# Optimization experiments

Measured on AMD Instinct MI355X. Metric: run time of the kernel, lower is better.

Reference implementation:

```python
import jax, jax.numpy as jnp
import numpy as np
import math

B, H, S, DK = 4, 16, 2048, 64

def setup_inputs() -> dict:
    key = jax.random.key(0)
    kq, kk, kv, km = jax.random.split(key, 4)
    q = jax.random.normal(kq, (B, H, S, DK), dtype=jnp.float32)
    k = jax.random.normal(kk, (B, H, S, DK), dtype=jnp.float32)
    v = jax.random.normal(kv, (B, H, S, DK), dtype=jnp.float32)
    mask = jax.random.randint(km, (B, 1, 1, S), 0, 2, dtype=jnp.int32)
    return {"q": q, "k": k, "v": v, "mask": mask}

def reference(q, k, v, mask):
    scale = 1.0 / math.sqrt(DK)
    # scores: [B, H, S, S]
    scores = jnp.einsum('bhqd,bhkd->bhqk', q, k) * scale
    scores = jnp.where(mask == 0, jnp.float32(-1e9), scores)
    attn = jax.nn.softmax(scores, axis=-1)
    out = jnp.einsum('bhqk,bhkd->bhqd', attn, v)
    return out
```

## Files before the change

### kernel.cpp

```cpp
#include <hip/hip_runtime.h>
#include <hip/hip_bf16.h>

#define S_LEN 2048
#define D_K   64
#define N_H   16
#define N_B   4
#define KVB   64
#define QPB   256
#define NQB   (S_LEN / QPB)
#define NBH   (N_B * N_H)
#define WS_NEED (2L * NBH * S_LEN * D_K * 2 + 4L * S_LEN * 4 + 16)

typedef __attribute__((ext_vector_type(8)))  short bf16x8;
typedef __attribute__((ext_vector_type(16))) float f32x16;
typedef unsigned int u32;
typedef __attribute__((ext_vector_type(4))) u32 u32x4;

__device__ inline short f2bfs(float x) {
    __hip_bfloat16 h = __float2bfloat16(x);
    return __builtin_bit_cast(short, h);
}

__device__ inline bf16x8 cvt8(const float* __restrict__ p) {
    float4 a = *(const float4*)p;
    float4 b = *(const float4*)(p + 4);
    bf16x8 f;
    f[0] = f2bfs(a.x); f[1] = f2bfs(a.y);
    f[2] = f2bfs(a.z); f[3] = f2bfs(a.w);
    f[4] = f2bfs(b.x); f[5] = f2bfs(b.y);
    f[6] = f2bfs(b.z); f[7] = f2bfs(b.w);
    return f;
}

__device__ inline bf16x8 cvt8s(const float* __restrict__ p, float s) {
    float4 a = *(const float4*)p;
    float4 b = *(const float4*)(p + 4);
    bf16x8 f;
    f[0] = f2bfs(a.x * s); f[1] = f2bfs(a.y * s);
    f[2] = f2bfs(a.z * s); f[3] = f2bfs(a.w * s);
    f[4] = f2bfs(b.x * s); f[5] = f2bfs(b.y * s);
    f[6] = f2bfs(b.z * s); f[7] = f2bfs(b.w * s);
    return f;
}

__device__ inline int vswz(int d) { return ((d & 7) ^ ((d >> 3) & 7)) << 4; }

__device__ inline void gld16(const void* g, void* l) {
    __builtin_amdgcn_global_load_lds(
        (const __attribute__((address_space(1))) void*)g,
        (__attribute__((address_space(3))) void*)l, 16, 0, 0);
}

__global__ __launch_bounds__(64)
void mask_scan(const int* __restrict__ mask, int* __restrict__ idx,
               int* __restrict__ cnt) {
    const int b = blockIdx.x, lane = threadIdx.x;
    const int* mb = mask + b * S_LEN;
    int base = 0;
    for (int j0 = 0; j0 < S_LEN; j0 += 64) {
        int mv = mb[j0 + lane];
        unsigned long long ball = __ballot(mv != 0);
        int pos = base + __popcll(ball & ((1ull << lane) - 1ull));
        if (mv) idx[b * S_LEN + pos] = j0 + lane;
        base += __popcll(ball);
    }
    if (lane == 0) cnt[b] = base;
}

__global__ __launch_bounds__(256)
void gather_cvt(const float* __restrict__ k, const float* __restrict__ v,
                const int* __restrict__ idx, const int* __restrict__ cnt,
                short* __restrict__ kc, short* __restrict__ vt) {
    const int bid = blockIdx.x, bh = bid >> 5, i0 = (bid & 31) * 64;
    const int b = bh >> 4;
    const int m = cnt[b];
    if (i0 >= ((m + 63) & ~63)) return;
    const int t = threadIdx.x;
    const int r = t >> 2, c0 = (t & 3) * 16;
    const int i = i0 + r;

    __shared__ __align__(16) short tile_[64][72];
    bf16x8 fv0, fv1, fk0, fk1;
    if (i < m) {
        const int src = idx[b * S_LEN + i];
        const float* kp = k + ((long)bh * S_LEN + src) * D_K + c0;
        const float* vp = v + ((long)bh * S_LEN + src) * D_K + c0;
        fk0 = cvt8(kp); fk1 = cvt8(kp + 8);
        fv0 = cvt8(vp); fv1 = cvt8(vp + 8);
    } else {
#pragma unroll
        for (int j = 0; j < 8; ++j) { fk0[j] = 0; fk1[j] = 0; fv0[j] = 0; fv1[j] = 0; }
    }
    short* kdst = kc + ((long)bh * S_LEN + i) * D_K + c0;
    *(bf16x8*)kdst       = fk0;
    *(bf16x8*)(kdst + 8) = fk1;
    *(bf16x8*)&tile_[r][c0]     = fv0;
    *(bf16x8*)&tile_[r][c0 + 8] = fv1;
    __syncthreads();
    const int dd = t >> 2, k0 = (t & 3) * 16;
    bf16x8 h0, h1;
#pragma unroll
    for (int j = 0; j < 8; ++j) {
        h0[j] = tile_[k0 + j][dd];
        h1[j] = tile_[k0 + 8 + j][dd];
    }
    short* dst = vt + ((long)bh * D_K + dd) * S_LEN + i0 + k0;
    *(bf16x8*)dst       = h0;
    *(bf16x8*)(dst + 8) = h1;
}

__global__ __launch_bounds__(512)
void attn_fwd(const float* __restrict__ q, const short* __restrict__ kbf,
              const short* __restrict__ vtb, const int* __restrict__ cnt,
              float* __restrict__ out) {
    const int id      = blockIdx.x;
    const int logical = (id & 7) * 64 + (id >> 3);
    const int bh      = logical >> 3;
    const int qblk    = logical & 7;
    const int b       = bh >> 4;
    const int t       = threadIdx.x;
    const int lane    = t & 63;
    const int wq      = t >> 6;
    const int hb      = lane >> 5;
    const int ql      = lane & 31;

    const int m   = cnt[b];
    const int NTr = (m + 63) >> 6;

    __shared__ __align__(16) short kbuf[5][KVB * D_K];
    __shared__ __align__(16) short vbuf[4][D_K * KVB];

    const float scale2 = 0.125f * 1.44269504f;
    const long  baseq  = (long)bh * S_LEN * D_K;
    const int   qrow0  = qblk * QPB + wq * 32;

    bf16x8 qf[4];
    {
        const float* qp = q + baseq + (long)(qrow0 + ql) * D_K + hb * 8;
#pragma unroll
        for (int kd = 0; kd < 4; ++kd) qf[kd] = cvt8s(qp + kd * 16, scale2);
    }

    const int lrow = lane >> 3, lchk = lane & 7;
    const int rA = wq * 8 + lrow;
    const short* ksA = kbf + baseq + (long)rA * D_K + ((lchk ^ (rA & 7)) * 8);
    const short* vsA = vtb + ((long)bh * D_K + rA) * S_LEN
                       + ((lchk ^ ((rA & 7) ^ ((rA >> 3) & 7))) * 8);

    auto STAGE_K = [&](int i) {
        gld16(ksA + (long)i * (KVB * D_K),
              (char*)kbuf + (i % 5) * (KVB * D_K * 2) + (wq * 8) * 128);
    };
    auto STAGE_V = [&](int i) {
        gld16(vsA + (long)i * KVB,
              (char*)vbuf + (i % 4) * (D_K * KVB * 2) + (wq * 8) * 128);
    };

    f32x16 o0, o1;
#pragma unroll
    for (int r = 0; r < 16; ++r) { o0[r] = 0.f; o1[r] = 0.f; }
    float lrun = 0.f;

    f32x16 ZEROV;
#pragma unroll
    for (int r = 0; r < 16; ++r) ZEROV[r] = 0.f;

    f32x16 st0, st1;

    auto QK = [&](int kv0, int sel, bool lastt) {
        const char* kbp = (const char*)kbuf + sel * (KVB * D_K * 2);
        int rb0 = (ql) * 128,      sz0 = (ql & 7) << 4;
        int rb1 = (32 + ql) * 128;
        f32x16 a0, a1;
        __builtin_amdgcn_s_setprio(1);
        {
            int co = (hb * 8) * 2;
            bf16x8 kf0 = *(const bf16x8*)(kbp + ((rb0 + co) ^ sz0));
            bf16x8 kf1 = *(const bf16x8*)(kbp + ((rb1 + co) ^ sz0));
            if (!lastt) {
                a0 = __builtin_amdgcn_mfma_f32_32x32x16_bf16(kf0, qf[0], ZEROV, 0, 0, 0);
                a1 = __builtin_amdgcn_mfma_f32_32x32x16_bf16(kf1, qf[0], ZEROV, 0, 0, 0);
            } else {
                f32x16 c0, c1;
                int keyb = kv0 + 4 * hb;
#pragma unroll
                for (int r = 0; r < 16; ++r) {
                    int key = keyb + (r & 3) + 8 * (r >> 2);
                    c0[r] = (key < m)      ? 0.f : -1e9f;
                    c1[r] = (key + 32 < m) ? 0.f : -1e9f;
                }
                a0 = __builtin_amdgcn_mfma_f32_32x32x16_bf16(kf0, qf[0], c0, 0, 0, 0);
                a1 = __builtin_amdgcn_mfma_f32_32x32x16_bf16(kf1, qf[0], c1, 0, 0, 0);
            }
        }
#pragma unroll
        for (int kd = 1; kd < 4; ++kd) {
            int co = (kd * 16 + hb * 8) * 2;
            bf16x8 kf0 = *(const bf16x8*)(kbp + ((rb0 + co) ^ sz0));
            bf16x8 kf1 = *(const bf16x8*)(kbp + ((rb1 + co) ^ sz0));
            a0 = __builtin_amdgcn_mfma_f32_32x32x16_bf16(kf0, qf[kd], a0, 0, 0, 0);
            a1 = __builtin_amdgcn_mfma_f32_32x32x16_bf16(kf1, qf[kd], a1, 0, 0, 0);
        }
        __builtin_amdgcn_s_setprio(0);
        st0 = a0; st1 = a1;
    };

    u32 w[2][8];

    auto SM = [&]() {
        float rs0 = 0.f, rs1 = 0.f;
#pragma unroll
        for (int mm = 0; mm < 8; ++mm) {
            float p0 = __builtin_amdgcn_exp2f(st0[2 * mm]);
            float p1 = __builtin_amdgcn_exp2f(st0[2 * mm + 1]);
            rs0 += p0; rs1 += p1;
            u32 r;
            asm("v_cvt_pk_bf16_f32 %0, %1, %2" : "=v"(r) : "v"(p0), "v"(p1));
            w[0][mm] = r;
        }
#pragma unroll
        for (int mm = 0; mm < 8; ++mm) {
            float p0 = __builtin_amdgcn_exp2f(st1[2 * mm]);
            float p1 = __builtin_amdgcn_exp2f(st1[2 * mm + 1]);
            rs0 += p0; rs1 += p1;
            u32 r;
            asm("v_cvt_pk_bf16_f32 %0, %1, %2" : "=v"(r) : "v"(p0), "v"(p1));
            w[1][mm] = r;
        }
        float rs = rs0 + rs1;
        rs += __shfl_xor(rs, 32, 64);
        lrun += rs;
    };

    auto PV = [&](int sel) {
        const char* vbp = (const char*)vbuf + sel * (D_K * KVB * 2);
#pragma unroll
        for (int kbi = 0; kbi < 4; ++kbi) {
            int c = kbi >> 1, a2 = (kbi & 1) * 4;
            u32 x0 = w[c][a2 + 0], y0 = w[c][a2 + 2];
            u32 x1 = w[c][a2 + 1], y1 = w[c][a2 + 3];
            asm("v_permlane32_swap_b32 %0, %1" : "+v"(x0), "+v"(y0));
            asm("v_permlane32_swap_b32 %0, %1" : "+v"(x1), "+v"(y1));
            u32x4 av = {x0, x1, y0, y1};
            bf16x8 pa = __builtin_bit_cast(bf16x8, av);
            __builtin_amdgcn_s_setprio(1);
#pragma unroll
            for (int dn = 0; dn < 2; ++dn) {
                int d = dn * 32 + ql;
                bf16x8 vf = *(const bf16x8*)(vbp +
                              ((d * 128 + (kbi * 16 + hb * 8) * 2) ^ vswz(d)));
                if (dn == 0)
                    o0 = __builtin_amdgcn_mfma_f32_32x32x16_bf16(pa, vf, o0, 0, 0, 0);
                else
                    o1 = __builtin_amdgcn_mfma_f32_32x32x16_bf16(pa, vf, o1, 0, 0, 0);
            }
            __builtin_amdgcn_s_setprio(0);
        }
    };

    STAGE_K(0);
    STAGE_V(0);
    if (NTr > 1) { STAGE_K(1); STAGE_V(1); }
    if (NTr > 2) STAGE_K(2);
    if (NTr > 3) STAGE_K(3);
    __syncthreads();
    QK(0, 0, NTr == 1);
    __syncthreads();

    for (int u = 0; 2 * u < NTr; ++u) {
        const int t0 = 2 * u, t1 = 2 * u + 1;
        if (t0 + 4 < NTr) STAGE_K(t0 + 4);
        if (t0 + 5 < NTr) STAGE_K(t0 + 5);
        if (t0 + 2 < NTr) STAGE_V(t0 + 2);
        if (t0 + 3 < NTr) STAGE_V(t0 + 3);

        SM();
        if (t0 + 1 < NTr) QK((t0 + 1) * KVB, (t0 + 1) % 5, t0 + 2 == NTr);
        PV(t0 & 3);

        if (t1 < NTr) {
            SM();
            if (t1 + 1 < NTr) QK((t1 + 1) * KVB, (t1 + 1) % 5, t1 + 2 == NTr);
            PV(t1 & 3);
        }

        __syncthreads();
    }

    float rl = 1.0f / lrun;
#pragma unroll
    for (int r = 0; r < 16; ++r) {
        int   cr  = (r & 3) + 8 * (r >> 2) + 4 * hb;
        float rlr = __shfl(rl, cr, 64);
        long  rowb = baseq + (long)(qrow0 + cr) * D_K;
        out[rowb + ql]      = o0[r] * rlr;
        out[rowb + 32 + ql] = o1[r] * rlr;
    }
}

__global__ __launch_bounds__(256)
void attn_fwd_legacy(const float* __restrict__ q, const float* __restrict__ k,
                     const float* __restrict__ v, const int* __restrict__ mask,
                     float* __restrict__ out) {
    const int id      = blockIdx.x;
    const int logical = (id & 7) * 128 + (id >> 3);
    const int bh      = logical >> 4;
    const int qblk    = logical & 15;
    const int b       = bh >> 4;
    const int t       = threadIdx.x;
    const int lane    = t & 63;
    const int wq      = t >> 6;
    const int hb      = lane >> 5;
    const int ql      = lane & 31;

    __shared__ __align__(16) short kbuf[KVB * D_K];
    __shared__ __align__(16) short vtbuf[D_K * KVB];
    __shared__ float mbias[S_LEN];

    const float scale2 = 0.125f * 1.44269504f;
    const long  base   = (long)bh * S_LEN * D_K;
    const int   qrow0  = qblk * 128 + wq * 32;

    {
        const int* mb = mask + b * S_LEN;
        for (int i = t; i < S_LEN; i += 256)
            mbias[i] = mb[i] ? 0.f : -1.442695e9f;
    }

    bf16x8 qf[4];
    {
        const float* qp = q + base + (long)(qrow0 + ql) * D_K + hb * 8;
#pragma unroll
        for (int kd = 0; kd < 4; ++kd) qf[kd] = cvt8s(qp + kd * 16, 1.0f);
    }

    f32x16 o0, o1;
#pragma unroll
    for (int r = 0; r < 16; ++r) { o0[r] = 0.f; o1[r] = 0.f; }
    float mrun = -1e30f, lrun = 0.f;

    const int srow = t >> 3;
    const int scol = t & 7;
    float4 kr[2][2], vr[2][2];

    auto LOADT = [&](int kv0) {
#pragma unroll
        for (int u2 = 0; u2 < 2; ++u2) {
            int row = srow + u2 * 32;
            const float* kp = k + base + (long)(kv0 + row) * D_K + scol * 8;
            const float* vp = v + base + (long)(kv0 + row) * D_K + scol * 8;
            kr[u2][0] = *(const float4*)kp; kr[u2][1] = *(const float4*)(kp + 4);
            vr[u2][0] = *(const float4*)vp; vr[u2][1] = *(const float4*)(vp + 4);
        }
    };

    LOADT(0);

    for (int tt = 0; tt < S_LEN / KVB; ++tt) {
        const int kv0 = tt * KVB;
        __syncthreads();
#pragma unroll
        for (int u2 = 0; u2 < 2; ++u2) {
            int row = srow + u2 * 32;
            bf16x8 fk, fv;
#pragma unroll
            for (int j = 0; j < 4; ++j) {
                fk[j]     = f2bfs(((const float*)&kr[u2][0])[j]);
                fk[j + 4] = f2bfs(((const float*)&kr[u2][1])[j]);
                fv[j]     = f2bfs(((const float*)&vr[u2][0])[j]);
                fv[j + 4] = f2bfs(((const float*)&vr[u2][1])[j]);
            }
            int kbyte = (row * 128 + scol * 16) ^ ((row & 7) << 4);
            *(bf16x8*)((char*)kbuf + kbyte) = fk;
#pragma unroll
            for (int j = 0; j < 8; ++j) {
                int d = scol * 8 + j;
                *(short*)((char*)vtbuf + ((d * 128 + row * 2) ^ vswz(d))) = fv[j];
            }
        }
        if (tt + 1 < S_LEN / KVB) LOADT(kv0 + KVB);
        __syncthreads();

        f32x16 stl[2];
#pragma unroll
        for (int kb32 = 0; kb32 < 2; ++kb32) {
            f32x16 acc;
#pragma unroll
            for (int r = 0; r < 16; ++r) acc[r] = 0.f;
            int krow = kb32 * 32 + ql;
            int rb = krow * 128, sz = (krow & 7) << 4;
#pragma unroll
            for (int kd = 0; kd < 4; ++kd) {
                bf16x8 kf = *(const bf16x8*)((const char*)kbuf + ((rb + (kd * 16 + hb * 8) * 2) ^ sz));
                acc = __builtin_amdgcn_mfma_f32_32x32x16_bf16(kf, qf[kd], acc, 0, 0, 0);
            }
            stl[kb32] = acc;
        }
#pragma unroll
        for (int kb32 = 0; kb32 < 2; ++kb32)
#pragma unroll
            for (int r = 0; r < 16; ++r) {
                int key = kv0 + kb32 * 32 + (r & 3) + 8 * (r >> 2) + 4 * hb;
                stl[kb32][r] = fmaf(stl[kb32][r], scale2, mbias[key]);
            }

        float m8[8];
#pragma unroll
        for (int i = 0; i < 8; ++i)
            m8[i] = fmaxf(fmaxf(stl[0][i], stl[0][i + 8]),
                          fmaxf(stl[1][i], stl[1][i + 8]));
        float tmax = fmaxf(fmaxf(fmaxf(m8[0], m8[1]), fmaxf(m8[2], m8[3])),
                           fmaxf(fmaxf(m8[4], m8[5]), fmaxf(m8[6], m8[7])));
        tmax = fmaxf(tmax, __shfl_xor(tmax, 32, 64));

        if (__any(tmax > mrun + 10.0f)) {
            float mnew = fmaxf(mrun, tmax);
            float al   = __builtin_amdgcn_exp2f(mrun - mnew);
            mrun = mnew;
            lrun *= al;
#pragma unroll
            for (int r = 0; r < 16; ++r) {
                float ar = __shfl(al, (r & 3) + 8 * (r >> 2) + 4 * hb, 64);
                o0[r] *= ar; o1[r] *= ar;
            }
        }

        u32 w[2][8];
        float rs = 0.f;
#pragma unroll
        for (int kb32 = 0; kb32 < 2; ++kb32)
#pragma unroll
            for (int mm = 0; mm < 8; ++mm) {
                float p0 = __builtin_amdgcn_exp2f(stl[kb32][2 * mm]     - mrun);
                float p1 = __builtin_amdgcn_exp2f(stl[kb32][2 * mm + 1] - mrun);
                rs += p0 + p1;
                w[kb32][mm] = (u32)(unsigned short)f2bfs(p0) |
                              ((u32)(unsigned short)f2bfs(p1) << 16);
            }
        rs += __shfl_xor(rs, 32, 64);
        lrun += rs;

#pragma unroll
        for (int kbi = 0; kbi < 4; ++kbi) {
            int c = kbi >> 1, a2 = (kbi & 1) * 4;
            u32 x0 = w[c][a2 + 0], y0 = w[c][a2 + 2];
            u32 x1 = w[c][a2 + 1], y1 = w[c][a2 + 3];
            asm("v_permlane32_swap_b32 %0, %1" : "+v"(x0), "+v"(y0));
            asm("v_permlane32_swap_b32 %0, %1" : "+v"(x1), "+v"(y1));
            u32x4 av = {x0, x1, y0, y1};
            bf16x8 pa = __builtin_bit_cast(bf16x8, av);
#pragma unroll
            for (int dn = 0; dn < 2; ++dn) {
                int d = dn * 32 + ql;
                bf16x8 vf = *(const bf16x8*)((const char*)vtbuf +
                              ((d * 128 + (kbi * 16 + hb * 8) * 2) ^ vswz(d)));
                if (dn == 0)
                    o0 = __builtin_amdgcn_mfma_f32_32x32x16_bf16(pa, vf, o0, 0, 0, 0);
                else
                    o1 = __builtin_amdgcn_mfma_f32_32x32x16_bf16(pa, vf, o1, 0, 0, 0);
            }
        }
    }

    float rl = 1.0f / lrun;
#pragma unroll
    for (int r = 0; r < 16; ++r) {
        int   cr  = (r & 3) + 8 * (r >> 2) + 4 * hb;
        float rlr = __shfl(rl, cr, 64);
        long  rowb = base + (long)(qrow0 + cr) * D_K;
        out[rowb + ql]      = o0[r] * rlr;
        out[rowb + 32 + ql] = o1[r] * rlr;
    }
}

extern "C" void kernel_launch(void* const* d_in, const int* in_sizes, int n_in,
                              void* d_out, int out_size, void* d_ws, size_t ws_size,
                              hipStream_t stream) {
    const float* q    = (const float*)d_in[0];
    const float* k    = (const float*)d_in[1];
    const float* v    = (const float*)d_in[2];
    const int*   mask = (const int*)d_in[3];
    float*       out  = (float*)d_out;

    if (ws_size >= (size_t)WS_NEED) {
        short* kc  = (short*)d_ws;
        short* vt  = kc + (long)NBH * S_LEN * D_K;
        int*   idx = (int*)(vt + (long)NBH * S_LEN * D_K);
        int*   cnt = idx + 4 * S_LEN;
        mask_scan<<<dim3(N_B), 64, 0, stream>>>(mask, idx, cnt);
        gather_cvt<<<dim3(NBH * (S_LEN / 64)), 256, 0, stream>>>(k, v, idx, cnt, kc, vt);
        attn_fwd<<<dim3(NQB * NBH), 512, 0, stream>>>(q, kc, vt, cnt, out);
    } else {
        attn_fwd_legacy<<<dim3((S_LEN / 128) * NBH), 256, 0, stream>>>(q, k, v, mask, out);
    }
}
```

Measured before the change: 80.80 us.

## Fuse mask compaction scan into gather kernel and defer row-sum shuffle

Removes the separate single-wave-per-batch mask_scan launch. Each gather_cvt block now rescans the mask itself and keeps only the 64 compacted indices it needs in shared memory. This saves a kernel launch and a serial dependency, at the cost of every block redundantly reading 2048 mask ints. Separately, the softmax row-sum cross-half shuffle is moved out of the per-tile loop and done once at the end.

```diff
diff --git a/kernel.cpp b/kernel.cpp
--- a/kernel.cpp
+++ b/kernel.cpp
@@ -51,38 +51,44 @@
         (__attribute__((address_space(3))) void*)l, 16, 0, 0);
 }
 
-__global__ __launch_bounds__(64)
-void mask_scan(const int* __restrict__ mask, int* __restrict__ idx,
-               int* __restrict__ cnt) {
-    const int b = blockIdx.x, lane = threadIdx.x;
-    const int* mb = mask + b * S_LEN;
-    int base = 0;
-    for (int j0 = 0; j0 < S_LEN; j0 += 64) {
-        int mv = mb[j0 + lane];
-        unsigned long long ball = __ballot(mv != 0);
-        int pos = base + __popcll(ball & ((1ull << lane) - 1ull));
-        if (mv) idx[b * S_LEN + pos] = j0 + lane;
-        base += __popcll(ball);
-    }
-    if (lane == 0) cnt[b] = base;
-}
-
 __global__ __launch_bounds__(256)
 void gather_cvt(const float* __restrict__ k, const float* __restrict__ v,
-                const int* __restrict__ idx, const int* __restrict__ cnt,
-                short* __restrict__ kc, short* __restrict__ vt) {
+                const int* __restrict__ mask, const int dummy,
+                short* __restrict__ kc, short* __restrict__ vt,
+                int* __restrict__ cnt) {
     const int bid = blockIdx.x, bh = bid >> 5, i0 = (bid & 31) * 64;
     const int b = bh >> 4;
-    const int m = cnt[b];
+    const int t = threadIdx.x;
+
+    __shared__ __align__(16) short tile_[64][72];
+    __shared__ int idx_s[64];
+    __shared__ int m_s;
+
+    if (t < 64) {
+        const int lane = t;
+        const int* mb = mask + b * S_LEN;
+        int base = 0;
+#pragma unroll 4
+        for (int j0 = 0; j0 < S_LEN; j0 += 64) {
+            int mv = mb[j0 + lane];
+            unsigned long long ball = __ballot(mv != 0);
+            int pos = base + __popcll(ball & ((1ull << lane) - 1ull));
+            if (mv && pos >= i0 && pos < i0 + 64) idx_s[pos - i0] = j0 + lane;
+            base += __popcll(ball);
+        }
+        if (lane == 0) m_s = base;
+    }
+    __syncthreads();
+    const int m = m_s;
+    if (t == 0 && i0 == 0) cnt[b] = m;
     if (i0 >= ((m + 63) & ~63)) return;
-    const int t = threadIdx.x;
+
     const int r = t >> 2, c0 = (t & 3) * 16;
     const int i = i0 + r;
 
-    __shared__ __align__(16) short tile_[64][72];
     bf16x8 fv0, fv1, fk0, fk1;
     if (i < m) {
-        const int src = idx[b * S_LEN + i];
+        const int src = idx_s[r];
         const float* kp = k + ((long)bh * S_LEN + src) * D_K + c0;
         const float* vp = v + ((long)bh * S_LEN + src) * D_K + c0;
         fk0 = cvt8(kp); fk1 = cvt8(kp + 8);
@@ -159,7 +165,7 @@
     f32x16 o0, o1;
 #pragma unroll
     for (int r = 0; r < 16; ++r) { o0[r] = 0.f; o1[r] = 0.f; }
-    float lrun = 0.f;
+    float lpart = 0.f;
 
     f32x16 ZEROV;
 #pragma unroll
@@ -227,9 +233,7 @@
             asm("v_cvt_pk_bf16_f32 %0, %1, %2" : "=v"(r) : "v"(p0), "v"(p1));
             w[1][mm] = r;
         }
-        float rs = rs0 + rs1;
-        rs += __shfl_xor(rs, 32, 64);
-        lrun += rs;
+        lpart += rs0 + rs1;
     };
 
     auto PV = [&](int sel) {
@@ -287,6 +291,7 @@
         __syncthreads();
     }
 
+    float lrun = lpart + __shfl_xor(lpart, 32, 64);
     float rl = 1.0f / lrun;
 #pragma unroll
     for (int r = 0; r < 16; ++r) {
@@ -485,10 +490,8 @@
     if (ws_size >= (size_t)WS_NEED) {
         short* kc  = (short*)d_ws;
         short* vt  = kc + (long)NBH * S_LEN * D_K;
-        int*   idx = (int*)(vt + (long)NBH * S_LEN * D_K);
-        int*   cnt = idx + 4 * S_LEN;
-        mask_scan<<<dim3(N_B), 64, 0, stream>>>(mask, idx, cnt);
-        gather_cvt<<<dim3(NBH * (S_LEN / 64)), 256, 0, stream>>>(k, v, idx, cnt, kc, vt);
+        int*   cnt = (int*)(vt + (long)NBH * S_LEN * D_K);
+        gather_cvt<<<dim3(NBH * (S_LEN / 64)), 256, 0, stream>>>(k, v, mask, 0, kc, vt, cnt);
         attn_fwd<<<dim3(NQB * NBH), 512, 0, stream>>>(q, kc, vt, cnt, out);
     } else {
         attn_fwd_legacy<<<dim3((S_LEN / 128) * NBH), 256, 0, stream>>>(q, k, v, mask, out);
```

After: 77.60 us (median of 2 runs). 4.0% less time.
